# Performance work log

Measured on AMD Instinct MI355X. Metric: run time of the kernel, lower is better.

## Reference

```python
import jax, jax.numpy as jnp
import numpy as np

B, M, N, D, C = 4, 256, 128, 512, 1024  # batch, enc frames, dec positions, d_model, n_classes
JOINT = 2 * D


def setup_inputs() -> dict:
    key = jax.random.key(0)
    ks = jax.random.split(key, 6)
    return {
        "enc_out": jax.random.normal(ks[0], (B, M, D), dtype=jnp.float32),
        "dec_out": jax.random.normal(ks[1], (B, N, D), dtype=jnp.float32),
        "w1": jax.random.normal(ks[2], (D, JOINT), dtype=jnp.float32) * (1.0 / np.sqrt(JOINT)),
        "b1": jax.random.normal(ks[3], (D,), dtype=jnp.float32) * 0.02,
        "w2": jax.random.normal(ks[4], (C, D), dtype=jnp.float32) * (1.0 / np.sqrt(D)),
        "b2": jax.random.normal(ks[5], (C,), dtype=jnp.float32) * 0.02,
    }


def reference(enc_out, dec_out, w1, b1, w2, b2):
    """RNN-T joint: log_softmax(fc2(tanh(fc1(cat(broadcast(enc), broadcast(dec)))))).

    fc1 on the concatenated [B,M,N,2D] tensor is computed equivalently as a
    broadcasted sum of two small matmuls, avoiding the materialized concat.
    """
    d = enc_out.shape[-1]
    w1_enc = w1[:, :d]  # [D, D] acts on encoder half of the concat
    w1_dec = w1[:, d:]  # [D, D] acts on decoder half
    he = jnp.einsum("bmd,ed->bme", enc_out, w1_enc)  # [B, M, D]
    hd = jnp.einsum("bnd,ed->bne", dec_out, w1_dec)  # [B, N, D]
    hid = jnp.tanh(he[:, :, None, :] + hd[:, None, :, :] + b1)  # [B, M, N, D]
    logits = jnp.einsum("bmne,ce->bmnc", hid, w2) + b2  # [B, M, N, C]
    return jax.nn.log_softmax(logits, axis=-1)
```

## Files before the change

### kernel.cpp

```cpp
#include <hip/hip_runtime.h>


typedef __attribute__((ext_vector_type(8))) __bf16 bf16x8;
typedef __attribute__((ext_vector_type(8))) unsigned short u16x8;
typedef __attribute__((ext_vector_type(4))) float f32x4;
typedef __attribute__((ext_vector_type(4))) int i32x4;
typedef __attribute__((ext_vector_type(16))) int i32x16;

__device__ __forceinline__ float tanh_fast(float x) {
    float e = __expf(2.0f * x);
    return 1.0f - 2.0f / (e + 1.0f);
}
__device__ __forceinline__ float bf2f(unsigned short u) {
    return __builtin_bit_cast(float, (unsigned)u << 16);
}
__device__ __forceinline__ unsigned short f2bf(float f) {
    return __builtin_bit_cast(unsigned short, (__bf16)f);
}
__device__ __forceinline__ int pack4(float a, float b, float c, float d, float s) {
    int q0 = __float2int_rn(a * s) & 255;
    int q1 = __float2int_rn(b * s) & 255;
    int q2 = __float2int_rn(c * s) & 255;
    int q3 = __float2int_rn(d * s) & 255;
    return q0 | (q1 << 8) | (q2 << 16) | (q3 << 24);
}

__device__ __forceinline__ int swz(int row, int kbyte) {
    return row * 1024 + (kbyte ^ ((row & 7) << 4));
}

__device__ __forceinline__ bf16x8 cvt8(float4 a, float4 b) {
    bf16x8 r;
    r[0] = (__bf16)a.x; r[1] = (__bf16)a.y; r[2] = (__bf16)a.z; r[3] = (__bf16)a.w;
    r[4] = (__bf16)b.x; r[5] = (__bf16)b.y; r[6] = (__bf16)b.z; r[7] = (__bf16)b.w;
    return r;
}

__global__ __launch_bounds__(512) void k_prep(
    const float* __restrict__ enc, const float* __restrict__ dec,
    const float* __restrict__ w1, const float* __restrict__ b1,
    const float* __restrict__ w2,
    float* __restrict__ heb, unsigned short* __restrict__ hdb,
    char* __restrict__ w2p, float* __restrict__ scF)
{
    const int bid = blockIdx.x, tid = threadIdx.x;
    const int lane = tid & 63, wid = tid >> 6;

    if (bid >= 48) {
        int W = (bid - 48) * 8 + wid;
        #pragma unroll
        for (int j = 0; j < 8; ++j) {
            int c = W * 8 + j;
            const float4* s = (const float4*)(w2 + c * 512 + lane * 8);
            float4 a = s[0], bq = s[1];
            float m = fmaxf(fmaxf(fabsf(a.x), fabsf(a.y)), fmaxf(fabsf(a.z), fabsf(a.w)));
            m = fmaxf(m, fmaxf(fmaxf(fabsf(bq.x), fabsf(bq.y)),
                               fmaxf(fabsf(bq.z), fabsf(bq.w))));
            #pragma unroll
            for (int d = 1; d < 64; d <<= 1) m = fmaxf(m, __shfl_xor(m, d));
            float r = 127.f / m;
            int d0 = pack4(a.x, a.y, a.z, a.w, r);
            int d1 = pack4(bq.x, bq.y, bq.z, bq.w, r);
            int t = lane >> 2, lhc = (lane >> 1) & 1, off = lane & 1;
            char* dst = w2p + ((size_t)((c >> 5) * 16 + t)) * 1024
                        + lhc * 512 + (c & 31) * 16 + off * 8;
            *(unsigned long long*)dst =
                (unsigned)d0 | ((unsigned long long)(unsigned)d1 << 32);
            if (lane == 0) scF[c] = m / 16129.f;
        }
        return;
    }

    __shared__ uint4 ldsq[2048];
    char* lds = (char*)ldsq;

    const bool ishe = bid < 32;
    const int r0 = (ishe ? bid : bid - 32) * 32;
    const float* src = (ishe ? enc : dec) + r0 * 512;
    const float* wsrc = w1 + (ishe ? 0 : 512);

    #pragma unroll
    for (int j = 0; j < 4; j++) {
        int row = wid * 4 + j;
        const float4* p = (const float4*)(src + row * 512 + lane * 8);
        *(bf16x8*)(lds + swz(row, lane * 16)) = cvt8(p[0], p[1]);
    }
    __syncthreads();

    const int lr = lane & 15, lg = lane >> 4;
    f32x4 acc[2][4];
    #pragma unroll
    for (int rt = 0; rt < 2; rt++)
        #pragma unroll
        for (int ct = 0; ct < 4; ct++)
            acc[rt][ct] = f32x4{0.f, 0.f, 0.f, 0.f};

    #pragma unroll 1
    for (int ks = 0; ks < 512; ks += 32) {
        bf16x8 af[2];
        #pragma unroll
        for (int rt = 0; rt < 2; rt++)
            af[rt] = *(const bf16x8*)(lds + swz(rt * 16 + lr, ks * 2 + lg * 16));
        #pragma unroll
        for (int ct = 0; ct < 4; ct++) {
            int col = wid * 64 + ct * 16 + lr;
            const float4* wp = (const float4*)(wsrc + col * 1024 + ks + lg * 8);
            bf16x8 bfr = cvt8(wp[0], wp[1]);
            #pragma unroll
            for (int rt = 0; rt < 2; rt++)
                acc[rt][ct] = __builtin_amdgcn_mfma_f32_16x16x32_bf16(af[rt], bfr, acc[rt][ct], 0, 0, 0);
        }
    }

    if (ishe) {
        float b1v[4];
        #pragma unroll
        for (int ct = 0; ct < 4; ct++) b1v[ct] = b1[wid * 64 + ct * 16 + lr];
        #pragma unroll
        for (int rt = 0; rt < 2; rt++)
            #pragma unroll
            for (int ct = 0; ct < 4; ct++)
                #pragma unroll
                for (int reg = 0; reg < 4; reg++)
                    heb[(r0 + rt * 16 + lg * 4 + reg) * 512 + wid * 64 + ct * 16 + lr] =
                        acc[rt][ct][reg] + b1v[ct];
    } else {
        #pragma unroll
        for (int rt = 0; rt < 2; rt++)
            #pragma unroll
            for (int ct = 0; ct < 4; ct++)
                #pragma unroll
                for (int reg = 0; reg < 4; reg++)
                    hdb[(r0 + rt * 16 + lg * 4 + reg) * 512 + wid * 64 + ct * 16 + lr] =
                        f2bf(acc[rt][ct][reg]);
    }
}

__global__ __launch_bounds__(512, 4) void k_main(
    const float* __restrict__ heb, const unsigned short* __restrict__ hdb,
    const float* __restrict__ b2, const char* __restrict__ w2p,
    const float* __restrict__ scF, float* __restrict__ out)
{
    __shared__ uint4 ldsq[2048];
    __shared__ float redm[32][8];
    __shared__ float reds[32][8];
    char* lds = (char*)ldsq;

    const int bid = ((blockIdx.x & 7) << 9) | (blockIdx.x >> 3);
    const int tid = threadIdx.x;
    const int bm = bid >> 2, nq = bid & 3;
    const int b = bm >> 8;
    const int lane = tid & 63, w = tid >> 6;
    const int l5 = lane & 31, lh = lane >> 5;

    {
        const unsigned short* hb = hdb + (size_t)(b * 128 + nq * 32 + l5) * 512;
        const float* ep = heb + (size_t)bm * 512;
        #pragma unroll
        for (int it = 0; it < 2; ++it) {
            int t = w * 2 + it;
            int k0 = t * 32 + lh * 16;
            u16x8 hv0 = *(const u16x8*)(hb + k0);
            u16x8 hv1 = *(const u16x8*)(hb + k0 + 8);
            float4 e0 = *(const float4*)(ep + k0);
            float4 e1 = *(const float4*)(ep + k0 + 4);
            float4 e2 = *(const float4*)(ep + k0 + 8);
            float4 e3 = *(const float4*)(ep + k0 + 12);
            i32x4 o;
            o[0] = pack4(tanh_fast(bf2f(hv0[0]) + e0.x), tanh_fast(bf2f(hv0[1]) + e0.y),
                         tanh_fast(bf2f(hv0[2]) + e0.z), tanh_fast(bf2f(hv0[3]) + e0.w), 127.f);
            o[1] = pack4(tanh_fast(bf2f(hv0[4]) + e1.x), tanh_fast(bf2f(hv0[5]) + e1.y),
                         tanh_fast(bf2f(hv0[6]) + e1.z), tanh_fast(bf2f(hv0[7]) + e1.w), 127.f);
            o[2] = pack4(tanh_fast(bf2f(hv1[0]) + e2.x), tanh_fast(bf2f(hv1[1]) + e2.y),
                         tanh_fast(bf2f(hv1[2]) + e2.z), tanh_fast(bf2f(hv1[3]) + e2.w), 127.f);
            o[3] = pack4(tanh_fast(bf2f(hv1[4]) + e3.x), tanh_fast(bf2f(hv1[5]) + e3.y),
                         tanh_fast(bf2f(hv1[6]) + e3.z), tanh_fast(bf2f(hv1[7]) + e3.w), 127.f);
            *(i32x4*)(lds + t * 1024 + lane * 16) = o;
        }
    }
    __syncthreads();

    const char* pw = w2p + ((size_t)w << 16) + (lane << 4);
    const char* la = lds + (lane << 4);

    i32x16 acc[4];
    #pragma unroll
    for (int ct = 0; ct < 4; ct++)
        #pragma unroll
        for (int r = 0; r < 16; r++)
            acc[ct][r] = 0;

    i32x4 aw[2][4];
    #pragma unroll
    for (int ct = 0; ct < 4; ct++) {
        aw[0][ct] = *(const i32x4*)(pw + ct * 16384);
        aw[1][ct] = *(const i32x4*)(pw + ct * 16384 + 1024);
    }
    i32x4 h0 = *(const i32x4*)(la);

    #pragma unroll
    for (int kt = 0; kt < 16; ++kt) {
        i32x4 hn;
        if (kt < 15) hn = *(const i32x4*)(la + (kt + 1) * 1024);
        __builtin_amdgcn_s_setprio(1);
        #pragma unroll
        for (int ct = 0; ct < 4; ct++)
            acc[ct] = __builtin_amdgcn_mfma_i32_32x32x32_i8(aw[kt & 1][ct], h0, acc[ct], 0, 0, 0);
        __builtin_amdgcn_s_setprio(0);
        if (kt < 14) {
            #pragma unroll
            for (int ct = 0; ct < 4; ct++)
                aw[kt & 1][ct] = *(const i32x4*)(pw + ct * 16384 + (kt + 2) * 1024);
        }
        h0 = hn;
    }

    #pragma unroll
    for (int ct = 0; ct < 4; ct++)
        #pragma unroll
        for (int q = 0; q < 4; q++) {
            const int base = w * 128 + ct * 32 + q * 8 + lh * 4;
            float4 sc4 = *(const float4*)(scF + base);
            float4 b24 = *(const float4*)(b2 + base);
            acc[ct][q * 4 + 0] = __float_as_int((float)acc[ct][q * 4 + 0] * sc4.x + b24.x);
            acc[ct][q * 4 + 1] = __float_as_int((float)acc[ct][q * 4 + 1] * sc4.y + b24.y);
            acc[ct][q * 4 + 2] = __float_as_int((float)acc[ct][q * 4 + 2] * sc4.z + b24.z);
            acc[ct][q * 4 + 3] = __float_as_int((float)acc[ct][q * 4 + 3] * sc4.w + b24.w);
        }

    float mx = -3.4e38f;
    #pragma unroll
    for (int ct = 0; ct < 4; ct++)
        #pragma unroll
        for (int r = 0; r < 16; r++)
            mx = fmaxf(mx, __int_as_float(acc[ct][r]));
    float sv = 0.f;
    #pragma unroll
    for (int ct = 0; ct < 4; ct++)
        #pragma unroll
        for (int r = 0; r < 16; r++)
            sv += __expf(__int_as_float(acc[ct][r]) - mx);
    {
        float mo = __shfl_xor(mx, 32), so = __shfl_xor(sv, 32);
        float mn = fmaxf(mx, mo);
        sv = sv * __expf(mx - mn) + so * __expf(mo - mn);
        mx = mn;
    }
    if (lh == 0) { redm[l5][w] = mx; reds[l5][w] = sv; }
    __syncthreads();

    float logZ;
    {
        float4 ma = *(const float4*)&redm[l5][0];
        float4 mb = *(const float4*)&redm[l5][4];
        float4 sa = *(const float4*)&reds[l5][0];
        float4 sb = *(const float4*)&reds[l5][4];
        float M = fmaxf(fmaxf(fmaxf(ma.x, ma.y), fmaxf(ma.z, ma.w)),
                        fmaxf(fmaxf(mb.x, mb.y), fmaxf(mb.z, mb.w)));
        float S = sa.x * __expf(ma.x - M) + sa.y * __expf(ma.y - M)
                + sa.z * __expf(ma.z - M) + sa.w * __expf(ma.w - M)
                + sb.x * __expf(mb.x - M) + sb.y * __expf(mb.y - M)
                + sb.z * __expf(mb.z - M) + sb.w * __expf(mb.w - M);
        logZ = M + __logf(S);
    }

    char* myr = lds + w * 4096;
    const size_t rowbase = (size_t)bm * 128 + nq * 32;
    const int rr = lane >> 2, c4 = lane & 3;
    #pragma unroll
    for (int ct = 0; ct < 4; ct++) {
        #pragma unroll
        for (int q = 0; q < 4; q++) {
            f32x4 o;
            o[0] = __int_as_float(acc[ct][q * 4 + 0]) - logZ;
            o[1] = __int_as_float(acc[ct][q * 4 + 1]) - logZ;
            o[2] = __int_as_float(acc[ct][q * 4 + 2]) - logZ;
            o[3] = __int_as_float(acc[ct][q * 4 + 3]) - logZ;
            *(f32x4*)(myr + l5 * 128 + ((q * 32 + lh * 16) ^ ((l5 & 7) << 4))) = o;
        }
        #pragma unroll
        for (int rh = 0; rh < 2; rh++)
            #pragma unroll
            for (int chv = 0; chv < 2; chv++) {
                int row = rh * 16 + rr;
                f32x4 v = *(const f32x4*)(myr + row * 128 +
                                          ((chv * 64 + c4 * 16) ^ ((row & 7) << 4)));
                __builtin_nontemporal_store(v,
                    (f32x4*)(out + (rowbase + row) * 1024 + w * 128 + ct * 32 +
                             chv * 16 + c4 * 4));
            }
    }
}

extern "C" void kernel_launch(void* const* d_in, const int* in_sizes, int n_in,
                              void* d_out, int out_size, void* d_ws, size_t ws_size,
                              hipStream_t stream) {
    const float* enc = (const float*)d_in[0];
    const float* dec = (const float*)d_in[1];
    const float* w1  = (const float*)d_in[2];
    const float* b1  = (const float*)d_in[3];
    const float* w2  = (const float*)d_in[4];
    const float* b2  = (const float*)d_in[5];

    float* heb = (float*)d_ws;
    unsigned short* hdb = (unsigned short*)(heb + 1024 * 512);
    char* w2p = (char*)(hdb + 512 * 512);
    float* scF = (float*)(w2p + 512 * 1024);

    k_prep<<<64, 512, 0, stream>>>(enc, dec, w1, b1, w2, heb, hdb, w2p, scF);
    k_main<<<4096, 512, 0, stream>>>(heb, hdb, b2, w2p, scF, (float*)d_out);
}
```

Before: 223.2 us.

## Double rows per block with 1024-thread blocks and 2x2 MFMA register tiles

Each block now handles 64 decoder rows instead of 32, using 16 waves. Each wave computes a 2x2 tile of 32x32 int8 MFMA outputs over 64 classes rather than 1x4 over 128. This halves the W2 traffic per output row and reuses each weight fragment across two row tiles, and the weight prefetch depth goes from 2 to 4 k-steps. In exchange it uses more LDS (a separate transpose buffer and larger reduction arrays), needs 1024-thread blocks, and cuts the grid to 2048 blocks, which may lower occupancy and raise register pressure.

```diff
diff --git a/kernel.cpp b/kernel.cpp
--- a/kernel.cpp
+++ b/kernel.cpp
@@ -136,32 +136,35 @@
     }
 }
 
-__global__ __launch_bounds__(512, 4) void k_main(
+__global__ __launch_bounds__(1024, 4) void k_main(
     const float* __restrict__ heb, const unsigned short* __restrict__ hdb,
     const float* __restrict__ b2, const char* __restrict__ w2p,
     const float* __restrict__ scF, float* __restrict__ out)
 {
-    __shared__ uint4 ldsq[2048];
-    __shared__ float redm[32][8];
-    __shared__ float reds[32][8];
-    char* lds = (char*)ldsq;
-
-    const int bid = ((blockIdx.x & 7) << 9) | (blockIdx.x >> 3);
+    __shared__ uint4 hidq[2048];
+    __shared__ uint4 trans[4096];
+    __shared__ float redm[64][16];
+    __shared__ float reds[64][16];
+    char* hid = (char*)hidq;
+
+    const int item = ((blockIdx.x & 7) << 8) | (blockIdx.x >> 3);
     const int tid = threadIdx.x;
-    const int bm = bid >> 2, nq = bid & 3;
+    const int bm = item >> 1, n0 = (item & 1) << 6;
     const int b = bm >> 8;
     const int lane = tid & 63, w = tid >> 6;
     const int l5 = lane & 31, lh = lane >> 5;
 
     {
-        const unsigned short* hb = hdb + (size_t)(b * 128 + nq * 32 + l5) * 512;
         const float* ep = heb + (size_t)bm * 512;
         #pragma unroll
         for (int it = 0; it < 2; ++it) {
-            int t = w * 2 + it;
+            int R = w * 2 + it;
+            int rt = R >> 4, t = R & 15;
             int k0 = t * 32 + lh * 16;
-            u16x8 hv0 = *(const u16x8*)(hb + k0);
-            u16x8 hv1 = *(const u16x8*)(hb + k0 + 8);
+            const unsigned short* hb =
+                hdb + (size_t)(b * 128 + n0 + rt * 32 + l5) * 512 + k0;
+            u16x8 hv0 = *(const u16x8*)(hb);
+            u16x8 hv1 = *(const u16x8*)(hb + 8);
             float4 e0 = *(const float4*)(ep + k0);
             float4 e1 = *(const float4*)(ep + k0 + 4);
             float4 e2 = *(const float4*)(ep + k0 + 8);
@@ -175,121 +178,153 @@
                          tanh_fast(bf2f(hv1[2]) + e2.z), tanh_fast(bf2f(hv1[3]) + e2.w), 127.f);
             o[3] = pack4(tanh_fast(bf2f(hv1[4]) + e3.x), tanh_fast(bf2f(hv1[5]) + e3.y),
                          tanh_fast(bf2f(hv1[6]) + e3.z), tanh_fast(bf2f(hv1[7]) + e3.w), 127.f);
-            *(i32x4*)(lds + t * 1024 + lane * 16) = o;
+            *(i32x4*)(hid + R * 1024 + lane * 16) = o;
         }
     }
     __syncthreads();
 
-    const char* pw = w2p + ((size_t)w << 16) + (lane << 4);
-    const char* la = lds + (lane << 4);
-
-    i32x16 acc[4];
-    #pragma unroll
-    for (int ct = 0; ct < 4; ct++)
-        #pragma unroll
-        for (int r = 0; r < 16; r++)
-            acc[ct][r] = 0;
-
-    i32x4 aw[2][4];
-    #pragma unroll
-    for (int ct = 0; ct < 4; ct++) {
-        aw[0][ct] = *(const i32x4*)(pw + ct * 16384);
-        aw[1][ct] = *(const i32x4*)(pw + ct * 16384 + 1024);
-    }
-    i32x4 h0 = *(const i32x4*)(la);
+    const char* pw = w2p + ((size_t)w << 15) + (lane << 4);
+    const char* la = hid + (lane << 4);
+
+    i32x16 acc[2][2];
+    #pragma unroll
+    for (int rt = 0; rt < 2; rt++)
+        #pragma unroll
+        for (int ct = 0; ct < 2; ct++)
+            #pragma unroll
+            for (int r = 0; r < 16; r++)
+                acc[rt][ct][r] = 0;
+
+    i32x4 aw[4][2];
+    #pragma unroll
+    for (int s = 0; s < 4; s++)
+        #pragma unroll
+        for (int ct = 0; ct < 2; ct++)
+            aw[s][ct] = *(const i32x4*)(pw + ct * 16384 + s * 1024);
+
+    i32x4 h0[2];
+    #pragma unroll
+    for (int rt = 0; rt < 2; rt++)
+        h0[rt] = *(const i32x4*)(la + rt * 16384);
 
     #pragma unroll
     for (int kt = 0; kt < 16; ++kt) {
-        i32x4 hn;
-        if (kt < 15) hn = *(const i32x4*)(la + (kt + 1) * 1024);
+        i32x4 hn[2];
+        if (kt < 15) {
+            #pragma unroll
+            for (int rt = 0; rt < 2; rt++)
+                hn[rt] = *(const i32x4*)(la + rt * 16384 + (kt + 1) * 1024);
+        }
         __builtin_amdgcn_s_setprio(1);
         #pragma unroll
-        for (int ct = 0; ct < 4; ct++)
-            acc[ct] = __builtin_amdgcn_mfma_i32_32x32x32_i8(aw[kt & 1][ct], h0, acc[ct], 0, 0, 0);
+        for (int ct = 0; ct < 2; ct++)
+            #pragma unroll
+            for (int rt = 0; rt < 2; rt++)
+                acc[rt][ct] = __builtin_amdgcn_mfma_i32_32x32x32_i8(
+                    aw[kt & 3][ct], h0[rt], acc[rt][ct], 0, 0, 0);
         __builtin_amdgcn_s_setprio(0);
-        if (kt < 14) {
-            #pragma unroll
-            for (int ct = 0; ct < 4; ct++)
-                aw[kt & 1][ct] = *(const i32x4*)(pw + ct * 16384 + (kt + 2) * 1024);
-        }
-        h0 = hn;
-    }
-
-    #pragma unroll
-    for (int ct = 0; ct < 4; ct++)
+        if (kt < 12) {
+            #pragma unroll
+            for (int ct = 0; ct < 2; ct++)
+                aw[kt & 3][ct] = *(const i32x4*)(pw + ct * 16384 + (kt + 4) * 1024);
+        }
+        h0[0] = hn[0]; h0[1] = hn[1];
+    }
+
+    #pragma unroll
+    for (int ct = 0; ct < 2; ct++)
         #pragma unroll
         for (int q = 0; q < 4; q++) {
-            const int base = w * 128 + ct * 32 + q * 8 + lh * 4;
+            const int base = w * 64 + ct * 32 + q * 8 + lh * 4;
             float4 sc4 = *(const float4*)(scF + base);
             float4 b24 = *(const float4*)(b2 + base);
-            acc[ct][q * 4 + 0] = __float_as_int((float)acc[ct][q * 4 + 0] * sc4.x + b24.x);
-            acc[ct][q * 4 + 1] = __float_as_int((float)acc[ct][q * 4 + 1] * sc4.y + b24.y);
-            acc[ct][q * 4 + 2] = __float_as_int((float)acc[ct][q * 4 + 2] * sc4.z + b24.z);
-            acc[ct][q * 4 + 3] = __float_as_int((float)acc[ct][q * 4 + 3] * sc4.w + b24.w);
-        }
-
-    float mx = -3.4e38f;
-    #pragma unroll
-    for (int ct = 0; ct < 4; ct++)
-        #pragma unroll
-        for (int r = 0; r < 16; r++)
-            mx = fmaxf(mx, __int_as_float(acc[ct][r]));
-    float sv = 0.f;
-    #pragma unroll
-    for (int ct = 0; ct < 4; ct++)
-        #pragma unroll
-        for (int r = 0; r < 16; r++)
-            sv += __expf(__int_as_float(acc[ct][r]) - mx);
-    {
+            #pragma unroll
+            for (int rt = 0; rt < 2; rt++) {
+                acc[rt][ct][q * 4 + 0] = __float_as_int((float)acc[rt][ct][q * 4 + 0] * sc4.x + b24.x);
+                acc[rt][ct][q * 4 + 1] = __float_as_int((float)acc[rt][ct][q * 4 + 1] * sc4.y + b24.y);
+                acc[rt][ct][q * 4 + 2] = __float_as_int((float)acc[rt][ct][q * 4 + 2] * sc4.z + b24.z);
+                acc[rt][ct][q * 4 + 3] = __float_as_int((float)acc[rt][ct][q * 4 + 3] * sc4.w + b24.w);
+            }
+        }
+
+    #pragma unroll
+    for (int rt = 0; rt < 2; rt++) {
+        float mx = -3.4e38f;
+        #pragma unroll
+        for (int ct = 0; ct < 2; ct++)
+            #pragma unroll
+            for (int r = 0; r < 16; r++)
+                mx = fmaxf(mx, __int_as_float(acc[rt][ct][r]));
+        float sv = 0.f;
+        #pragma unroll
+        for (int ct = 0; ct < 2; ct++)
+            #pragma unroll
+            for (int r = 0; r < 16; r++)
+                sv += __expf(__int_as_float(acc[rt][ct][r]) - mx);
         float mo = __shfl_xor(mx, 32), so = __shfl_xor(sv, 32);
         float mn = fmaxf(mx, mo);
         sv = sv * __expf(mx - mn) + so * __expf(mo - mn);
         mx = mn;
-    }
-    if (lh == 0) { redm[l5][w] = mx; reds[l5][w] = sv; }
+        if (lh == 0) {
+            redm[rt * 32 + l5][w] = mx;
+            reds[rt * 32 + l5][w] = sv;
+        }
+    }
     __syncthreads();
 
-    float logZ;
-    {
-        float4 ma = *(const float4*)&redm[l5][0];
-        float4 mb = *(const float4*)&redm[l5][4];
-        float4 sa = *(const float4*)&reds[l5][0];
-        float4 sb = *(const float4*)&reds[l5][4];
-        float M = fmaxf(fmaxf(fmaxf(ma.x, ma.y), fmaxf(ma.z, ma.w)),
-                        fmaxf(fmaxf(mb.x, mb.y), fmaxf(mb.z, mb.w)));
-        float S = sa.x * __expf(ma.x - M) + sa.y * __expf(ma.y - M)
-                + sa.z * __expf(ma.z - M) + sa.w * __expf(ma.w - M)
-                + sb.x * __expf(mb.x - M) + sb.y * __expf(mb.y - M)
-                + sb.z * __expf(mb.z - M) + sb.w * __expf(mb.w - M);
-        logZ = M + __logf(S);
-    }
-
-    char* myr = lds + w * 4096;
-    const size_t rowbase = (size_t)bm * 128 + nq * 32;
+    float logZ[2];
+    #pragma unroll
+    for (int rt = 0; rt < 2; rt++) {
+        int r = rt * 32 + l5;
+        const float4* mp = (const float4*)&redm[r][0];
+        const float4* sp = (const float4*)&reds[r][0];
+        float M;
+        {
+            float4 m0 = mp[0], m1 = mp[1], m2 = mp[2], m3 = mp[3];
+            float a0 = fmaxf(fmaxf(m0.x, m0.y), fmaxf(m0.z, m0.w));
+            float a1 = fmaxf(fmaxf(m1.x, m1.y), fmaxf(m1.z, m1.w));
+            float a2 = fmaxf(fmaxf(m2.x, m2.y), fmaxf(m2.z, m2.w));
+            float a3 = fmaxf(fmaxf(m3.x, m3.y), fmaxf(m3.z, m3.w));
+            M = fmaxf(fmaxf(a0, a1), fmaxf(a2, a3));
+        }
+        float S = 0.f;
+        #pragma unroll
+        for (int q = 0; q < 4; q++) {
+            float4 mq = mp[q], sq = sp[q];
+            S += sq.x * __expf(mq.x - M) + sq.y * __expf(mq.y - M)
+               + sq.z * __expf(mq.z - M) + sq.w * __expf(mq.w - M);
+        }
+        logZ[rt] = M + __logf(S);
+    }
+
+    char* myr = (char*)trans + w * 4096;
+    const size_t rowbase = (size_t)bm * 128 + n0;
     const int rr = lane >> 2, c4 = lane & 3;
     #pragma unroll
-    for (int ct = 0; ct < 4; ct++) {
-        #pragma unroll
-        for (int q = 0; q < 4; q++) {
-            f32x4 o;
-            o[0] = __int_as_float(acc[ct][q * 4 + 0]) - logZ;
-            o[1] = __int_as_float(acc[ct][q * 4 + 1]) - logZ;
-            o[2] = __int_as_float(acc[ct][q * 4 + 2]) - logZ;
-            o[3] = __int_as_float(acc[ct][q * 4 + 3]) - logZ;
-            *(f32x4*)(myr + l5 * 128 + ((q * 32 + lh * 16) ^ ((l5 & 7) << 4))) = o;
-        }
-        #pragma unroll
-        for (int rh = 0; rh < 2; rh++)
-            #pragma unroll
-            for (int chv = 0; chv < 2; chv++) {
-                int row = rh * 16 + rr;
-                f32x4 v = *(const f32x4*)(myr + row * 128 +
-                                          ((chv * 64 + c4 * 16) ^ ((row & 7) << 4)));
-                __builtin_nontemporal_store(v,
-                    (f32x4*)(out + (rowbase + row) * 1024 + w * 128 + ct * 32 +
-                             chv * 16 + c4 * 4));
+    for (int rt = 0; rt < 2; rt++)
+        #pragma unroll
+        for (int ct = 0; ct < 2; ct++) {
+            #pragma unroll
+            for (int q = 0; q < 4; q++) {
+                f32x4 o;
+                o[0] = __int_as_float(acc[rt][ct][q * 4 + 0]) - logZ[rt];
+                o[1] = __int_as_float(acc[rt][ct][q * 4 + 1]) - logZ[rt];
+                o[2] = __int_as_float(acc[rt][ct][q * 4 + 2]) - logZ[rt];
+                o[3] = __int_as_float(acc[rt][ct][q * 4 + 3]) - logZ[rt];
+                *(f32x4*)(myr + l5 * 128 + ((q * 32 + lh * 16) ^ ((l5 & 7) << 4))) = o;
             }
-    }
+            #pragma unroll
+            for (int rh = 0; rh < 2; rh++)
+                #pragma unroll
+                for (int chv = 0; chv < 2; chv++) {
+                    int row = rh * 16 + rr;
+                    f32x4 v = *(const f32x4*)(myr + row * 128 +
+                                              ((chv * 64 + c4 * 16) ^ ((row & 7) << 4)));
+                    __builtin_nontemporal_store(v,
+                        (f32x4*)(out + (rowbase + rt * 32 + row) * 1024 + w * 64 +
+                                 ct * 32 + chv * 16 + c4 * 4));
+                }
+        }
 }
 
 extern "C" void kernel_launch(void* const* d_in, const int* in_sizes, int n_in,
@@ -308,5 +343,5 @@
     float* scF = (float*)(w2p + 512 * 1024);
 
     k_prep<<<64, 512, 0, stream>>>(enc, dec, w1, b1, w2, heb, hdb, w2p, scF);
-    k_main<<<4096, 512, 0, stream>>>(heb, hdb, b2, w2p, scF, (float*)d_out);
-}
+    k_main<<<2048, 1024, 0, stream>>>(heb, hdb, b2, w2p, scF, (float*)d_out);
+}
```

Result: slower. 305.0 us (+36.7%).

## Make k_main persistent over 16 tiles with prefetch and double-buffered LDS

Applied to the files above, without the earlier changes.

The main kernel now launches 256 blocks, each looping over 16 work items instead of one item per block. It prefetches the next item's he/hd inputs into registers during the current item's epilogue and alternates between two LDS hidden-state buffers. The W2 register prefetch depth grows from 2 to 4 k-steps, and launch bounds drop to 2 blocks per CU. The goal is to amortise block launch and prologue cost and to overlap global loads with compute and stores, at the price of fewer resident blocks per CU and a smaller per-warp store staging area.

```diff
diff --git a/kernel.cpp b/kernel.cpp
--- a/kernel.cpp
+++ b/kernel.cpp
@@ -23,6 +23,12 @@
     int q2 = __float2int_rn(c * s) & 255;
     int q3 = __float2int_rn(d * s) & 255;
     return q0 | (q1 << 8) | (q2 << 16) | (q3 << 24);
+}
+
+__device__ __forceinline__ void barrier_lgkm() {
+    asm volatile("s_waitcnt lgkmcnt(0)" ::: "memory");
+    __builtin_amdgcn_s_barrier();
+    asm volatile("" ::: "memory");
 }
 
 __device__ __forceinline__ int swz(int row, int kbyte) {
@@ -136,158 +142,189 @@
     }
 }
 
-__global__ __launch_bounds__(512, 4) void k_main(
+__device__ __forceinline__ void issue_stage(
+    int item, const float* heb, const unsigned short* hdb,
+    int w, int l5, int lh, u16x8 (&Hv)[2][2], float4 (&Ev)[2][4])
+{
+    const int bm = item >> 2, nq = item & 3, bq = bm >> 8;
+    const float* ep = heb + (size_t)bm * 512;
+    #pragma unroll
+    for (int it = 0; it < 2; ++it) {
+        int k0 = (w * 2 + it) * 32 + lh * 16;
+        const unsigned short* hb = hdb + (size_t)(bq * 128 + nq * 32 + l5) * 512 + k0;
+        Hv[it][0] = *(const u16x8*)hb;
+        Hv[it][1] = *(const u16x8*)(hb + 8);
+        Ev[it][0] = *(const float4*)(ep + k0);
+        Ev[it][1] = *(const float4*)(ep + k0 + 4);
+        Ev[it][2] = *(const float4*)(ep + k0 + 8);
+        Ev[it][3] = *(const float4*)(ep + k0 + 12);
+    }
+}
+
+__global__ __launch_bounds__(512, 2) void k_main(
     const float* __restrict__ heb, const unsigned short* __restrict__ hdb,
     const float* __restrict__ b2, const char* __restrict__ w2p,
     const float* __restrict__ scF, float* __restrict__ out)
 {
-    __shared__ uint4 ldsq[2048];
+    __shared__ uint4 hidq[2][1024];
     __shared__ float redm[32][8];
     __shared__ float reds[32][8];
-    char* lds = (char*)ldsq;
-
-    const int bid = ((blockIdx.x & 7) << 9) | (blockIdx.x >> 3);
+
+    const int bid = ((blockIdx.x & 7) << 5) | (blockIdx.x >> 3);
     const int tid = threadIdx.x;
-    const int bm = bid >> 2, nq = bid & 3;
-    const int b = bm >> 8;
     const int lane = tid & 63, w = tid >> 6;
     const int l5 = lane & 31, lh = lane >> 5;
 
-    {
-        const unsigned short* hb = hdb + (size_t)(b * 128 + nq * 32 + l5) * 512;
-        const float* ep = heb + (size_t)bm * 512;
+    const char* pw = w2p + ((size_t)w << 16) + (lane << 4);
+    const int rr = lane >> 2, c4 = lane & 3;
+
+    u16x8 Hv[2][2];
+    float4 Ev[2][4];
+    issue_stage(bid * 16, heb, hdb, w, l5, lh, Hv, Ev);
+
+    #pragma unroll 1
+    for (int j = 0; j < 16; ++j) {
+        const int item = bid * 16 + j;
+        const int bm = item >> 2, nq = item & 3;
+        char* hid = (char*)&hidq[j & 1][0];
+
         #pragma unroll
         for (int it = 0; it < 2; ++it) {
             int t = w * 2 + it;
-            int k0 = t * 32 + lh * 16;
-            u16x8 hv0 = *(const u16x8*)(hb + k0);
-            u16x8 hv1 = *(const u16x8*)(hb + k0 + 8);
-            float4 e0 = *(const float4*)(ep + k0);
-            float4 e1 = *(const float4*)(ep + k0 + 4);
-            float4 e2 = *(const float4*)(ep + k0 + 8);
-            float4 e3 = *(const float4*)(ep + k0 + 12);
             i32x4 o;
-            o[0] = pack4(tanh_fast(bf2f(hv0[0]) + e0.x), tanh_fast(bf2f(hv0[1]) + e0.y),
-                         tanh_fast(bf2f(hv0[2]) + e0.z), tanh_fast(bf2f(hv0[3]) + e0.w), 127.f);
-            o[1] = pack4(tanh_fast(bf2f(hv0[4]) + e1.x), tanh_fast(bf2f(hv0[5]) + e1.y),
-                         tanh_fast(bf2f(hv0[6]) + e1.z), tanh_fast(bf2f(hv0[7]) + e1.w), 127.f);
-            o[2] = pack4(tanh_fast(bf2f(hv1[0]) + e2.x), tanh_fast(bf2f(hv1[1]) + e2.y),
-                         tanh_fast(bf2f(hv1[2]) + e2.z), tanh_fast(bf2f(hv1[3]) + e2.w), 127.f);
-            o[3] = pack4(tanh_fast(bf2f(hv1[4]) + e3.x), tanh_fast(bf2f(hv1[5]) + e3.y),
-                         tanh_fast(bf2f(hv1[6]) + e3.z), tanh_fast(bf2f(hv1[7]) + e3.w), 127.f);
-            *(i32x4*)(lds + t * 1024 + lane * 16) = o;
-        }
-    }
-    __syncthreads();
-
-    const char* pw = w2p + ((size_t)w << 16) + (lane << 4);
-    const char* la = lds + (lane << 4);
-
-    i32x16 acc[4];
-    #pragma unroll
-    for (int ct = 0; ct < 4; ct++)
-        #pragma unroll
-        for (int r = 0; r < 16; r++)
-            acc[ct][r] = 0;
-
-    i32x4 aw[2][4];
-    #pragma unroll
-    for (int ct = 0; ct < 4; ct++) {
-        aw[0][ct] = *(const i32x4*)(pw + ct * 16384);
-        aw[1][ct] = *(const i32x4*)(pw + ct * 16384 + 1024);
-    }
-    i32x4 h0 = *(const i32x4*)(la);
-
-    #pragma unroll
-    for (int kt = 0; kt < 16; ++kt) {
-        i32x4 hn;
-        if (kt < 15) hn = *(const i32x4*)(la + (kt + 1) * 1024);
-        __builtin_amdgcn_s_setprio(1);
-        #pragma unroll
-        for (int ct = 0; ct < 4; ct++)
-            acc[ct] = __builtin_amdgcn_mfma_i32_32x32x32_i8(aw[kt & 1][ct], h0, acc[ct], 0, 0, 0);
-        __builtin_amdgcn_s_setprio(0);
-        if (kt < 14) {
+            o[0] = pack4(tanh_fast(bf2f(Hv[it][0][0]) + Ev[it][0].x),
+                         tanh_fast(bf2f(Hv[it][0][1]) + Ev[it][0].y),
+                         tanh_fast(bf2f(Hv[it][0][2]) + Ev[it][0].z),
+                         tanh_fast(bf2f(Hv[it][0][3]) + Ev[it][0].w), 127.f);
+            o[1] = pack4(tanh_fast(bf2f(Hv[it][0][4]) + Ev[it][1].x),
+                         tanh_fast(bf2f(Hv[it][0][5]) + Ev[it][1].y),
+                         tanh_fast(bf2f(Hv[it][0][6]) + Ev[it][1].z),
+                         tanh_fast(bf2f(Hv[it][0][7]) + Ev[it][1].w), 127.f);
+            o[2] = pack4(tanh_fast(bf2f(Hv[it][1][0]) + Ev[it][2].x),
+                         tanh_fast(bf2f(Hv[it][1][1]) + Ev[it][2].y),
+                         tanh_fast(bf2f(Hv[it][1][2]) + Ev[it][2].z),
+                         tanh_fast(bf2f(Hv[it][1][3]) + Ev[it][2].w), 127.f);
+            o[3] = pack4(tanh_fast(bf2f(Hv[it][1][4]) + Ev[it][3].x),
+                         tanh_fast(bf2f(Hv[it][1][5]) + Ev[it][3].y),
+                         tanh_fast(bf2f(Hv[it][1][6]) + Ev[it][3].z),
+                         tanh_fast(bf2f(Hv[it][1][7]) + Ev[it][3].w), 127.f);
+            *(i32x4*)(hid + t * 1024 + lane * 16) = o;
+        }
+        barrier_lgkm();
+
+        const char* la = hid + (lane << 4);
+
+        i32x16 acc[4];
+        #pragma unroll
+        for (int ct = 0; ct < 4; ct++)
+            #pragma unroll
+            for (int r = 0; r < 16; r++)
+                acc[ct][r] = 0;
+
+        i32x4 aw[4][4];
+        #pragma unroll
+        for (int s = 0; s < 4; s++)
             #pragma unroll
             for (int ct = 0; ct < 4; ct++)
-                aw[kt & 1][ct] = *(const i32x4*)(pw + ct * 16384 + (kt + 2) * 1024);
-        }
-        h0 = hn;
-    }
-
-    #pragma unroll
-    for (int ct = 0; ct < 4; ct++)
-        #pragma unroll
-        for (int q = 0; q < 4; q++) {
-            const int base = w * 128 + ct * 32 + q * 8 + lh * 4;
-            float4 sc4 = *(const float4*)(scF + base);
-            float4 b24 = *(const float4*)(b2 + base);
-            acc[ct][q * 4 + 0] = __float_as_int((float)acc[ct][q * 4 + 0] * sc4.x + b24.x);
-            acc[ct][q * 4 + 1] = __float_as_int((float)acc[ct][q * 4 + 1] * sc4.y + b24.y);
-            acc[ct][q * 4 + 2] = __float_as_int((float)acc[ct][q * 4 + 2] * sc4.z + b24.z);
-            acc[ct][q * 4 + 3] = __float_as_int((float)acc[ct][q * 4 + 3] * sc4.w + b24.w);
-        }
-
-    float mx = -3.4e38f;
-    #pragma unroll
-    for (int ct = 0; ct < 4; ct++)
-        #pragma unroll
-        for (int r = 0; r < 16; r++)
-            mx = fmaxf(mx, __int_as_float(acc[ct][r]));
-    float sv = 0.f;
-    #pragma unroll
-    for (int ct = 0; ct < 4; ct++)
-        #pragma unroll
-        for (int r = 0; r < 16; r++)
-            sv += __expf(__int_as_float(acc[ct][r]) - mx);
-    {
-        float mo = __shfl_xor(mx, 32), so = __shfl_xor(sv, 32);
-        float mn = fmaxf(mx, mo);
-        sv = sv * __expf(mx - mn) + so * __expf(mo - mn);
-        mx = mn;
-    }
-    if (lh == 0) { redm[l5][w] = mx; reds[l5][w] = sv; }
-    __syncthreads();
-
-    float logZ;
-    {
-        float4 ma = *(const float4*)&redm[l5][0];
-        float4 mb = *(const float4*)&redm[l5][4];
-        float4 sa = *(const float4*)&reds[l5][0];
-        float4 sb = *(const float4*)&reds[l5][4];
-        float M = fmaxf(fmaxf(fmaxf(ma.x, ma.y), fmaxf(ma.z, ma.w)),
-                        fmaxf(fmaxf(mb.x, mb.y), fmaxf(mb.z, mb.w)));
-        float S = sa.x * __expf(ma.x - M) + sa.y * __expf(ma.y - M)
-                + sa.z * __expf(ma.z - M) + sa.w * __expf(ma.w - M)
-                + sb.x * __expf(mb.x - M) + sb.y * __expf(mb.y - M)
-                + sb.z * __expf(mb.z - M) + sb.w * __expf(mb.w - M);
-        logZ = M + __logf(S);
-    }
-
-    char* myr = lds + w * 4096;
-    const size_t rowbase = (size_t)bm * 128 + nq * 32;
-    const int rr = lane >> 2, c4 = lane & 3;
-    #pragma unroll
-    for (int ct = 0; ct < 4; ct++) {
-        #pragma unroll
-        for (int q = 0; q < 4; q++) {
-            f32x4 o;
-            o[0] = __int_as_float(acc[ct][q * 4 + 0]) - logZ;
-            o[1] = __int_as_float(acc[ct][q * 4 + 1]) - logZ;
-            o[2] = __int_as_float(acc[ct][q * 4 + 2]) - logZ;
-            o[3] = __int_as_float(acc[ct][q * 4 + 3]) - logZ;
-            *(f32x4*)(myr + l5 * 128 + ((q * 32 + lh * 16) ^ ((l5 & 7) << 4))) = o;
-        }
-        #pragma unroll
-        for (int rh = 0; rh < 2; rh++)
-            #pragma unroll
-            for (int chv = 0; chv < 2; chv++) {
-                int row = rh * 16 + rr;
-                f32x4 v = *(const f32x4*)(myr + row * 128 +
-                                          ((chv * 64 + c4 * 16) ^ ((row & 7) << 4)));
-                __builtin_nontemporal_store(v,
-                    (f32x4*)(out + (rowbase + row) * 1024 + w * 128 + ct * 32 +
-                             chv * 16 + c4 * 4));
+                aw[s][ct] = *(const i32x4*)(pw + ct * 16384 + s * 1024);
+        i32x4 h0 = *(const i32x4*)(la);
+
+        #pragma unroll
+        for (int kt = 0; kt < 16; ++kt) {
+            i32x4 hn = h0;
+            if (kt < 15) hn = *(const i32x4*)(la + (kt + 1) * 1024);
+            __builtin_amdgcn_s_setprio(1);
+            #pragma unroll
+            for (int ct = 0; ct < 4; ct++)
+                acc[ct] = __builtin_amdgcn_mfma_i32_32x32x32_i8(
+                    aw[kt & 3][ct], h0, acc[ct], 0, 0, 0);
+            __builtin_amdgcn_s_setprio(0);
+            if (kt < 12) {
+                #pragma unroll
+                for (int ct = 0; ct < 4; ct++)
+                    aw[kt & 3][ct] = *(const i32x4*)(pw + ct * 16384 + (kt + 4) * 1024);
+            }
+            h0 = hn;
+        }
+
+        #pragma unroll
+        for (int ct = 0; ct < 4; ct++)
+            #pragma unroll
+            for (int q = 0; q < 4; q++) {
+                const int base = w * 128 + ct * 32 + q * 8 + lh * 4;
+                float4 sc4 = *(const float4*)(scF + base);
+                float4 b24 = *(const float4*)(b2 + base);
+                acc[ct][q * 4 + 0] = __float_as_int((float)acc[ct][q * 4 + 0] * sc4.x + b24.x);
+                acc[ct][q * 4 + 1] = __float_as_int((float)acc[ct][q * 4 + 1] * sc4.y + b24.y);
+                acc[ct][q * 4 + 2] = __float_as_int((float)acc[ct][q * 4 + 2] * sc4.z + b24.z);
+                acc[ct][q * 4 + 3] = __float_as_int((float)acc[ct][q * 4 + 3] * sc4.w + b24.w);
+            }
+
+        float mx = -3.4e38f;
+        #pragma unroll
+        for (int ct = 0; ct < 4; ct++)
+            #pragma unroll
+            for (int r = 0; r < 16; r++)
+                mx = fmaxf(mx, __int_as_float(acc[ct][r]));
+        float sv = 0.f;
+        #pragma unroll
+        for (int ct = 0; ct < 4; ct++)
+            #pragma unroll
+            for (int r = 0; r < 16; r++)
+                sv += __expf(__int_as_float(acc[ct][r]) - mx);
+        {
+            float mo = __shfl_xor(mx, 32), so = __shfl_xor(sv, 32);
+            float mn = fmaxf(mx, mo);
+            sv = sv * __expf(mx - mn) + so * __expf(mo - mn);
+            mx = mn;
+        }
+        if (lh == 0) { redm[l5][w] = mx; reds[l5][w] = sv; }
+        barrier_lgkm();
+
+        float logZ;
+        {
+            float4 ma = *(const float4*)&redm[l5][0];
+            float4 mb = *(const float4*)&redm[l5][4];
+            float4 sa = *(const float4*)&reds[l5][0];
+            float4 sb = *(const float4*)&reds[l5][4];
+            float M = fmaxf(fmaxf(fmaxf(ma.x, ma.y), fmaxf(ma.z, ma.w)),
+                            fmaxf(fmaxf(mb.x, mb.y), fmaxf(mb.z, mb.w)));
+            float S = sa.x * __expf(ma.x - M) + sa.y * __expf(ma.y - M)
+                    + sa.z * __expf(ma.z - M) + sa.w * __expf(ma.w - M)
+                    + sb.x * __expf(mb.x - M) + sb.y * __expf(mb.y - M)
+                    + sb.z * __expf(mb.z - M) + sb.w * __expf(mb.w - M);
+            logZ = M + __logf(S);
+        }
+
+        if (j < 15)
+            issue_stage(item + 1, heb, hdb, w, l5, lh, Hv, Ev);
+        asm volatile("" ::: "memory");
+
+        char* myr = hid + w * 2048;
+        const size_t rowbase = (size_t)bm * 128 + nq * 32;
+        #pragma unroll
+        for (int ct = 0; ct < 4; ct++)
+            #pragma unroll
+            for (int qh = 0; qh < 2; qh++) {
+                #pragma unroll
+                for (int qi = 0; qi < 2; qi++) {
+                    int q = qh * 2 + qi;
+                    f32x4 o;
+                    o[0] = __int_as_float(acc[ct][q * 4 + 0]) - logZ;
+                    o[1] = __int_as_float(acc[ct][q * 4 + 1]) - logZ;
+                    o[2] = __int_as_float(acc[ct][q * 4 + 2]) - logZ;
+                    o[3] = __int_as_float(acc[ct][q * 4 + 3]) - logZ;
+                    *(f32x4*)(myr + l5 * 64 + ((qi * 32 + lh * 16) ^ ((l5 & 3) << 4))) = o;
+                }
+                #pragma unroll
+                for (int rh = 0; rh < 2; rh++) {
+                    int row = rh * 16 + rr;
+                    f32x4 v = *(const f32x4*)(myr + row * 64 +
+                                              ((c4 * 16) ^ ((row & 3) << 4)));
+                    __builtin_nontemporal_store(v,
+                        (f32x4*)(out + (rowbase + row) * 1024 + w * 128 + ct * 32 +
+                                 qh * 16 + c4 * 4));
+                }
             }
     }
 }
@@ -308,5 +345,5 @@
     float* scF = (float*)(w2p + 512 * 1024);
 
     k_prep<<<64, 512, 0, stream>>>(enc, dec, w1, b1, w2, heb, hdb, w2p, scF);
-    k_main<<<4096, 512, 0, stream>>>(heb, hdb, b2, w2p, scF, (float*)d_out);
-}
+    k_main<<<256, 512, 0, stream>>>(heb, hdb, b2, w2p, scF, (float*)d_out);
+}
```

After: 453.9 us. 2.03x slower.

## Stage decoder rows in LDS with coalesced loads and double prep grid

Applied to the files above, without the earlier changes.

In k_main, the block's 32 decoder rows of hdb are now loaded cooperatively into swizzled LDS with coalesced 16-byte loads, replacing the per-lane strided global reads. The tanh and quantize step then reads from LDS, holds the packed results in registers and writes them back after an extra barrier. k_prep now runs 128 blocks, each handling 16 rows instead of 32, to spread the small prep matmul over more CUs. The cost is two more __syncthreads per main block and less register reuse of A fragments in prep.

```diff
diff --git a/kernel.cpp b/kernel.cpp
--- a/kernel.cpp
+++ b/kernel.cpp
@@ -46,11 +46,11 @@
     const int bid = blockIdx.x, tid = threadIdx.x;
     const int lane = tid & 63, wid = tid >> 6;
 
-    if (bid >= 48) {
-        int W = (bid - 48) * 8 + wid;
-        #pragma unroll
-        for (int j = 0; j < 8; ++j) {
-            int c = W * 8 + j;
+    if (bid >= 96) {
+        int W = (bid - 96) * 8 + wid;
+        #pragma unroll
+        for (int j = 0; j < 4; ++j) {
+            int c = W * 4 + j;
             const float4* s = (const float4*)(w2 + c * 512 + lane * 8);
             float4 a = s[0], bq = s[1];
             float m = fmaxf(fmaxf(fabsf(a.x), fabsf(a.y)), fmaxf(fabsf(a.z), fabsf(a.w)));
@@ -71,44 +71,37 @@
         return;
     }
 
-    __shared__ uint4 ldsq[2048];
+    __shared__ uint4 ldsq[1024];
     char* lds = (char*)ldsq;
 
-    const bool ishe = bid < 32;
-    const int r0 = (ishe ? bid : bid - 32) * 32;
+    const bool ishe = bid < 64;
+    const int r0 = (ishe ? bid : bid - 64) * 16;
     const float* src = (ishe ? enc : dec) + r0 * 512;
     const float* wsrc = w1 + (ishe ? 0 : 512);
 
     #pragma unroll
-    for (int j = 0; j < 4; j++) {
-        int row = wid * 4 + j;
+    for (int j = 0; j < 2; j++) {
+        int row = wid * 2 + j;
         const float4* p = (const float4*)(src + row * 512 + lane * 8);
         *(bf16x8*)(lds + swz(row, lane * 16)) = cvt8(p[0], p[1]);
     }
     __syncthreads();
 
     const int lr = lane & 15, lg = lane >> 4;
-    f32x4 acc[2][4];
-    #pragma unroll
-    for (int rt = 0; rt < 2; rt++)
-        #pragma unroll
-        for (int ct = 0; ct < 4; ct++)
-            acc[rt][ct] = f32x4{0.f, 0.f, 0.f, 0.f};
+    f32x4 acc[4];
+    #pragma unroll
+    for (int ct = 0; ct < 4; ct++)
+        acc[ct] = f32x4{0.f, 0.f, 0.f, 0.f};
 
     #pragma unroll 1
     for (int ks = 0; ks < 512; ks += 32) {
-        bf16x8 af[2];
-        #pragma unroll
-        for (int rt = 0; rt < 2; rt++)
-            af[rt] = *(const bf16x8*)(lds + swz(rt * 16 + lr, ks * 2 + lg * 16));
+        bf16x8 af = *(const bf16x8*)(lds + swz(lr, ks * 2 + lg * 16));
         #pragma unroll
         for (int ct = 0; ct < 4; ct++) {
             int col = wid * 64 + ct * 16 + lr;
             const float4* wp = (const float4*)(wsrc + col * 1024 + ks + lg * 8);
             bf16x8 bfr = cvt8(wp[0], wp[1]);
-            #pragma unroll
-            for (int rt = 0; rt < 2; rt++)
-                acc[rt][ct] = __builtin_amdgcn_mfma_f32_16x16x32_bf16(af[rt], bfr, acc[rt][ct], 0, 0, 0);
+            acc[ct] = __builtin_amdgcn_mfma_f32_16x16x32_bf16(af, bfr, acc[ct], 0, 0, 0);
         }
     }
 
@@ -117,22 +110,18 @@
         #pragma unroll
         for (int ct = 0; ct < 4; ct++) b1v[ct] = b1[wid * 64 + ct * 16 + lr];
         #pragma unroll
-        for (int rt = 0; rt < 2; rt++)
-            #pragma unroll
-            for (int ct = 0; ct < 4; ct++)
-                #pragma unroll
-                for (int reg = 0; reg < 4; reg++)
-                    heb[(r0 + rt * 16 + lg * 4 + reg) * 512 + wid * 64 + ct * 16 + lr] =
-                        acc[rt][ct][reg] + b1v[ct];
+        for (int ct = 0; ct < 4; ct++)
+            #pragma unroll
+            for (int reg = 0; reg < 4; reg++)
+                heb[(r0 + lg * 4 + reg) * 512 + wid * 64 + ct * 16 + lr] =
+                    acc[ct][reg] + b1v[ct];
     } else {
         #pragma unroll
-        for (int rt = 0; rt < 2; rt++)
-            #pragma unroll
-            for (int ct = 0; ct < 4; ct++)
-                #pragma unroll
-                for (int reg = 0; reg < 4; reg++)
-                    hdb[(r0 + rt * 16 + lg * 4 + reg) * 512 + wid * 64 + ct * 16 + lr] =
-                        f2bf(acc[rt][ct][reg]);
+        for (int ct = 0; ct < 4; ct++)
+            #pragma unroll
+            for (int reg = 0; reg < 4; reg++)
+                hdb[(r0 + lg * 4 + reg) * 512 + wid * 64 + ct * 16 + lr] =
+                    f2bf(acc[ct][reg]);
     }
 }
 
@@ -154,30 +143,44 @@
     const int l5 = lane & 31, lh = lane >> 5;
 
     {
-        const unsigned short* hb = hdb + (size_t)(b * 128 + nq * 32 + l5) * 512;
+        const unsigned short* src = hdb + (size_t)(b * 128 + nq * 32) * 512;
+        #pragma unroll
+        for (int i = 0; i < 4; ++i) {
+            int o = tid * 4 + i;
+            int row = o >> 6, c16 = o & 63;
+            u16x8 v = *(const u16x8*)(src + row * 512 + c16 * 8);
+            *(u16x8*)(lds + swz(row, c16 * 16)) = v;
+        }
+    }
+    __syncthreads();
+
+    i32x4 oq[2];
+    {
         const float* ep = heb + (size_t)bm * 512;
         #pragma unroll
         for (int it = 0; it < 2; ++it) {
-            int t = w * 2 + it;
-            int k0 = t * 32 + lh * 16;
-            u16x8 hv0 = *(const u16x8*)(hb + k0);
-            u16x8 hv1 = *(const u16x8*)(hb + k0 + 8);
+            int k0 = (w * 2 + it) * 32 + lh * 16;
+            u16x8 hv0 = *(const u16x8*)(lds + swz(l5, k0 * 2));
+            u16x8 hv1 = *(const u16x8*)(lds + swz(l5, k0 * 2 + 16));
             float4 e0 = *(const float4*)(ep + k0);
             float4 e1 = *(const float4*)(ep + k0 + 4);
             float4 e2 = *(const float4*)(ep + k0 + 8);
             float4 e3 = *(const float4*)(ep + k0 + 12);
-            i32x4 o;
-            o[0] = pack4(tanh_fast(bf2f(hv0[0]) + e0.x), tanh_fast(bf2f(hv0[1]) + e0.y),
-                         tanh_fast(bf2f(hv0[2]) + e0.z), tanh_fast(bf2f(hv0[3]) + e0.w), 127.f);
-            o[1] = pack4(tanh_fast(bf2f(hv0[4]) + e1.x), tanh_fast(bf2f(hv0[5]) + e1.y),
-                         tanh_fast(bf2f(hv0[6]) + e1.z), tanh_fast(bf2f(hv0[7]) + e1.w), 127.f);
-            o[2] = pack4(tanh_fast(bf2f(hv1[0]) + e2.x), tanh_fast(bf2f(hv1[1]) + e2.y),
-                         tanh_fast(bf2f(hv1[2]) + e2.z), tanh_fast(bf2f(hv1[3]) + e2.w), 127.f);
-            o[3] = pack4(tanh_fast(bf2f(hv1[4]) + e3.x), tanh_fast(bf2f(hv1[5]) + e3.y),
-                         tanh_fast(bf2f(hv1[6]) + e3.z), tanh_fast(bf2f(hv1[7]) + e3.w), 127.f);
-            *(i32x4*)(lds + t * 1024 + lane * 16) = o;
-        }
-    }
+            oq[it][0] = pack4(tanh_fast(bf2f(hv0[0]) + e0.x), tanh_fast(bf2f(hv0[1]) + e0.y),
+                              tanh_fast(bf2f(hv0[2]) + e0.z), tanh_fast(bf2f(hv0[3]) + e0.w), 127.f);
+            oq[it][1] = pack4(tanh_fast(bf2f(hv0[4]) + e1.x), tanh_fast(bf2f(hv0[5]) + e1.y),
+                              tanh_fast(bf2f(hv0[6]) + e1.z), tanh_fast(bf2f(hv0[7]) + e1.w), 127.f);
+            oq[it][2] = pack4(tanh_fast(bf2f(hv1[0]) + e2.x), tanh_fast(bf2f(hv1[1]) + e2.y),
+                              tanh_fast(bf2f(hv1[2]) + e2.z), tanh_fast(bf2f(hv1[3]) + e2.w), 127.f);
+            oq[it][3] = pack4(tanh_fast(bf2f(hv1[4]) + e3.x), tanh_fast(bf2f(hv1[5]) + e3.y),
+                              tanh_fast(bf2f(hv1[6]) + e3.z), tanh_fast(bf2f(hv1[7]) + e3.w), 127.f);
+        }
+    }
+    __syncthreads();
+
+    #pragma unroll
+    for (int it = 0; it < 2; ++it)
+        *(i32x4*)(lds + (w * 2 + it) * 1024 + lane * 16) = oq[it];
     __syncthreads();
 
     const char* pw = w2p + ((size_t)w << 16) + (lane << 4);
@@ -200,7 +203,7 @@
 
     #pragma unroll
     for (int kt = 0; kt < 16; ++kt) {
-        i32x4 hn;
+        i32x4 hn = h0;
         if (kt < 15) hn = *(const i32x4*)(la + (kt + 1) * 1024);
         __builtin_amdgcn_s_setprio(1);
         #pragma unroll
@@ -307,6 +310,6 @@
     char* w2p = (char*)(hdb + 512 * 512);
     float* scF = (float*)(w2p + 512 * 1024);
 
-    k_prep<<<64, 512, 0, stream>>>(enc, dec, w1, b1, w2, heb, hdb, w2p, scF);
+    k_prep<<<128, 512, 0, stream>>>(enc, dec, w1, b1, w2, heb, hdb, w2p, scF);
     k_main<<<4096, 512, 0, stream>>>(heb, hdb, b2, w2p, scF, (float*)d_out);
 }
```

New measurement: 219.6 us. No clear change (-1.6%).
